# Kernel optimization log

Measured on AMD Instinct MI355X. Metric: run time of the kernel, lower is better.

Reference implementation:

```python
import jax, jax.numpy as jnp
import numpy as np

B, D, H = 16384, 1024, 4096


def setup_inputs() -> dict:
    key = jax.random.key(0)
    kx, kp, k1, k2 = jax.random.split(key, 4)
    X = jax.random.normal(kx, (B, D), dtype=jnp.float32)
    prot_col_idx = 3
    # protected column must be binary {0,1} so the remap produces no NaNs
    prot = jax.random.randint(kp, (B,), 0, 2).astype(jnp.float32)
    X = X.at[:, prot_col_idx].set(prot)
    W1 = jax.random.normal(k1, (D, H), dtype=jnp.float32) * (1.0 / np.sqrt(D))
    b1 = jnp.zeros((H,), dtype=jnp.float32)
    W2 = jax.random.normal(k2, (H, D), dtype=jnp.float32) * (1.0 / np.sqrt(H))
    b2 = jnp.zeros((D,), dtype=jnp.float32)
    return {"X": X, "W1": W1, "b1": b1, "W2": W2, "b2": b2,
            "prot_col_idx": prot_col_idx}


def reference(X, W1, b1, W2, b2, prot_col_idx):
    def explainer(x):
        h = jnp.tanh(x @ W1 + b1)          # [B, H]
        return h @ W2 + b2                  # [B, D]

    # vectorized remap of the protected column: 0 -> 1, 1 -> 0, else NaN
    col = X[:, prot_col_idx]
    flipped = jnp.where(col == 0, jnp.float32(1.0),
                        jnp.where(col == 1, jnp.float32(0.0), jnp.float32(jnp.nan)))
    X_copy = X.at[:, prot_col_idx].set(flipped.astype(X.dtype))

    shaps = explainer(X)
    shaps_counter = explainer(X_copy)
    mean_euclid_dist = jnp.mean(jnp.abs(shaps - shaps_counter), axis=0)  # [D]
    return mean_euclid_dist.sum()
```

## Files before the change

kernel.cpp:

```cpp
#include <hip/hip_runtime.h>
#include <stdint.h>

#define B_N 16384
#define D_N 1024
#define H_N 4096

typedef int i32x4 __attribute__((ext_vector_type(4)));
typedef int i32x8 __attribute__((ext_vector_type(8)));
typedef float f32x4 __attribute__((ext_vector_type(4)));

__device__ __forceinline__ void gload16(const void* g, void* l) {
  __builtin_amdgcn_global_load_lds((const __attribute__((address_space(1))) void*)g,
                                   (__attribute__((address_space(3))) void*)l,
                                   16, 0, 0);
}

__device__ __forceinline__ unsigned char f2fp8(float v) {
  return (unsigned char)(__builtin_amdgcn_cvt_pk_fp8_f32(v, v, 0, false) & 0xFF);
}

__global__ void pack_X_kernel(const float4* __restrict__ X4,
                              int* __restrict__ Xb,
                              float* __restrict__ s,
                              const int* __restrict__ pci_p) {
  int i = blockIdx.x * 256 + threadIdx.x;
  if (i >= B_N * (D_N / 4)) return;
  float4 v = X4[i];
  int p = __builtin_amdgcn_cvt_pk_fp8_f32(v.x, v.y, 0, false);
  p = __builtin_amdgcn_cvt_pk_fp8_f32(v.z, v.w, p, true);
  Xb[i] = p;
  int pci = *pci_p;
  int colg = i & (D_N / 4 - 1);
  if (colg == (pci >> 2)) {
    int row = i >> 8;
    float c;
    switch (pci & 3) {
      case 0:  c = v.x; break;
      case 1:  c = v.y; break;
      case 2:  c = v.z; break;
      default: c = v.w; break;
    }
    s[row] = 1.0f - 2.0f * c;
  }
}

__global__ void transpose_pack_fp8(const float* __restrict__ in,
                                   unsigned char* __restrict__ out,
                                   int R, int C, float scale,
                                   float* __restrict__ w3,
                                   const int* __restrict__ pci_p) {
  __shared__ float tile[32][33];
  int i0 = blockIdx.y * 32;
  int j0 = blockIdx.x * 32;
  int tx = threadIdx.x, ty = threadIdx.y;
  int pci = pci_p ? *pci_p : -1;
#pragma unroll
  for (int r = 0; r < 32; r += 8) {
    int i = i0 + ty + r;
    int j = j0 + tx;
    float v = in[(size_t)i * C + j];
    tile[ty + r][tx] = v;
    if (w3 != nullptr && i == pci) w3[j] = v;
  }
  __syncthreads();
#pragma unroll
  for (int r = 0; r < 32; r += 8) {
    int jo = j0 + ty + r;
    int io = i0 + tx;
    out[(size_t)jo * R + io] = f2fp8(tile[tx][ty + r] * scale);
  }
}

template <int KTOT>
__device__ __forceinline__ void mx_mainloop(
    const unsigned char* __restrict__ A, const unsigned char* __restrict__ B,
    int m0, int n0, int sa, int sb,
    unsigned char* As, unsigned char* Bs, f32x4 (&acc)[4][4]) {
  const int tid = threadIdx.x;
  const int lane = tid & 63;
  const int wave = tid >> 6;
  const int wm = (wave >> 1) * 64;
  const int wn = (wave & 1) * 64;
  const int lm = lane & 15;
  const int quad = lane >> 4;

  const int srow = tid >> 3;
  const int clog = (tid & 7) ^ (srow & 7);
  const unsigned char* Ag = A + (size_t)(m0 + srow) * KTOT + clog * 16;
  const unsigned char* Bg = B + (size_t)(n0 + srow) * KTOT + clog * 16;
  unsigned char* As_l = As + tid * 16;
  unsigned char* Bs_l = Bs + tid * 16;

  for (int k0 = 0; k0 < KTOT; k0 += 128) {
#pragma unroll
    for (int it = 0; it < 4; it++) {
      gload16(Ag + k0 + (size_t)(32 * it) * KTOT, As_l + it * 4096);
      gload16(Bg + k0 + (size_t)(32 * it) * KTOT, Bs_l + it * 4096);
    }
    __syncthreads();
    i32x8 a[4], b[4];
#pragma unroll
    for (int i = 0; i < 4; i++) {
      int r = wm + i * 16 + lm;
      int e = r & 7;
      i32x4 lo = *(const i32x4*)&As[r * 128 + ((2 * quad) ^ e) * 16];
      i32x4 hi = *(const i32x4*)&As[r * 128 + ((2 * quad + 1) ^ e) * 16];
      a[i][0] = lo[0]; a[i][1] = lo[1]; a[i][2] = lo[2]; a[i][3] = lo[3];
      a[i][4] = hi[0]; a[i][5] = hi[1]; a[i][6] = hi[2]; a[i][7] = hi[3];
    }
#pragma unroll
    for (int j = 0; j < 4; j++) {
      int r = wn + j * 16 + lm;
      int e = r & 7;
      i32x4 lo = *(const i32x4*)&Bs[r * 128 + ((2 * quad) ^ e) * 16];
      i32x4 hi = *(const i32x4*)&Bs[r * 128 + ((2 * quad + 1) ^ e) * 16];
      b[j][0] = lo[0]; b[j][1] = lo[1]; b[j][2] = lo[2]; b[j][3] = lo[3];
      b[j][4] = hi[0]; b[j][5] = hi[1]; b[j][6] = hi[2]; b[j][7] = hi[3];
    }
#pragma unroll
    for (int i = 0; i < 4; i++)
#pragma unroll
      for (int j = 0; j < 4; j++)
        acc[i][j] = __builtin_amdgcn_mfma_scale_f32_16x16x128_f8f6f4(
            a[i], b[j], acc[i][j], 0, 0, 0, sa, 0, sb);
    __syncthreads();
  }
}

__device__ __forceinline__ void xcd_remap(int NT, int MT, int& m_t, int& n_t) {
  int l = blockIdx.y * NT + blockIdx.x;
  int x = l & 7;
  int k = l >> 3;
  m_t = x * (MT >> 3) + k / NT;
  n_t = k % NT;
}

__global__ __launch_bounds__(256) void gemm1_dh(
    const unsigned char* __restrict__ Xb,
    const unsigned char* __restrict__ W1T,
    const float* __restrict__ b1,
    const float* __restrict__ w3,
    const float* __restrict__ s,
    unsigned char* __restrict__ Dh) {
  __shared__ alignas(16) unsigned char As[128 * 128];
  __shared__ alignas(16) unsigned char Bs[128 * 128];
  int m_t, n_t;
  xcd_remap(H_N / 128, B_N / 128, m_t, n_t);
  const int m0 = m_t * 128, n0 = n_t * 128;

  f32x4 acc[4][4] = {};
  mx_mainloop<D_N>(Xb, W1T, m0, n0, 127, 123, As, Bs, acc);

  const int tid = threadIdx.x;
  const int lane = tid & 63;
  const int wave = tid >> 6;
  const int wm = (wave >> 1) * 64;
  const int wn = (wave & 1) * 64;
  const int lm = lane & 15;
  const int quad = lane >> 4;

  float ewp[4], ewm[4], b1v[4];
  int ghv[4];
#pragma unroll
  for (int j = 0; j < 4; j++) {
    int gh = n0 + wn + j * 16 + lm;
    float w = w3[gh];
    ewp[j] = __expf(2.0f * w);
    ewm[j] = __expf(-2.0f * w);
    b1v[j] = b1[gh];
    ghv[j] = gh;
  }
#pragma unroll
  for (int i = 0; i < 4; i++) {
#pragma unroll
    for (int r = 0; r < 4; r++) {
      int gb = m0 + wm + i * 16 + quad * 4 + r;
      float sv = s[gb];
      size_t rowbase = (size_t)gb * H_N;
#pragma unroll
      for (int j = 0; j < 4; j++) {
        float z = acc[i][j][r] + b1v[j];
        z = fminf(fmaxf(z, -20.0f), 20.0f);
        float E = __expf(2.0f * z);
        float ews = (sv > 0.0f) ? ewp[j] : ewm[j];
        float num = 2.0f * E * (1.0f - ews);
        float den = (E * ews + 1.0f) * (E + 1.0f);
        float dh = num * __builtin_amdgcn_rcpf(den);
        Dh[rowbase + ghv[j]] = f2fp8(dh * 64.0f);
      }
    }
  }
}

__global__ __launch_bounds__(256) void gemm2_abs(
    const unsigned char* __restrict__ Dh,
    const unsigned char* __restrict__ W2T,
    float* __restrict__ accum) {
  __shared__ alignas(16) unsigned char As[128 * 128];
  __shared__ alignas(16) unsigned char Bs[128 * 128];
  __shared__ float wsum[4];
  int m_t, n_t;
  xcd_remap(D_N / 128, B_N / 128, m_t, n_t);
  const int m0 = m_t * 128, n0 = n_t * 128;

  f32x4 acc[4][4] = {};
  mx_mainloop<H_N>(Dh, W2T, m0, n0, 121, 121, As, Bs, acc);

  const int tid = threadIdx.x;
  const int lane = tid & 63;
  const int wave = tid >> 6;

  float t = 0.0f;
#pragma unroll
  for (int i = 0; i < 4; i++)
#pragma unroll
    for (int j = 0; j < 4; j++)
#pragma unroll
      for (int r = 0; r < 4; r++)
        t += fabsf(acc[i][j][r]);

#pragma unroll
  for (int off2 = 32; off2 > 0; off2 >>= 1)
    t += __shfl_down(t, off2, 64);
  if (lane == 0) wsum[wave] = t;
  __syncthreads();
  if (tid == 0) atomicAdd(accum, wsum[0] + wsum[1] + wsum[2] + wsum[3]);
}

__global__ void finalize_kernel(const float* __restrict__ acc, float* __restrict__ out) {
  out[0] = acc[0] * (1.0f / (float)B_N);
}

extern "C" void kernel_launch(void* const* d_in, const int* in_sizes, int n_in,
                              void* d_out, int out_size, void* d_ws, size_t ws_size,
                              hipStream_t stream) {
  const float* X  = (const float*)d_in[0];
  const float* W1 = (const float*)d_in[1];
  const float* b1 = (const float*)d_in[2];
  const float* W2 = (const float*)d_in[3];
  const int* pci  = (const int*)d_in[5];

  char* ws = (char*)d_ws;
  size_t off = 0;
  unsigned char* Xb  = (unsigned char*)(ws + off); off += (size_t)B_N * D_N;
  unsigned char* W1T = (unsigned char*)(ws + off); off += (size_t)H_N * D_N;
  unsigned char* W2T = (unsigned char*)(ws + off); off += (size_t)D_N * H_N;
  float* w3  = (float*)(ws + off); off += (size_t)H_N * 4;
  float* s   = (float*)(ws + off); off += (size_t)B_N * 4;
  float* acc = (float*)(ws + off); off += 256;
  unsigned char* Dh  = (unsigned char*)(ws + off); off += (size_t)B_N * H_N;
  if (ws_size < off) return;

  hipMemsetAsync(acc, 0, sizeof(float), stream);
  pack_X_kernel<<<B_N * (D_N / 4) / 256, 256, 0, stream>>>((const float4*)X, (int*)Xb, s, pci);
  transpose_pack_fp8<<<dim3(H_N / 32, D_N / 32), dim3(32, 8), 0, stream>>>(W1, W1T, D_N, H_N, 16.0f, w3, pci);
  transpose_pack_fp8<<<dim3(D_N / 32, H_N / 32), dim3(32, 8), 0, stream>>>(W2, W2T, H_N, D_N, 64.0f, nullptr, nullptr);
  gemm1_dh<<<dim3(H_N / 128, B_N / 128), 256, 0, stream>>>(Xb, W1T, b1, w3, s, Dh);
  gemm2_abs<<<dim3(D_N / 128, B_N / 128), 256, 0, stream>>>(Dh, W2T, acc);
  finalize_kernel<<<1, 1, 0, stream>>>(acc, (float*)d_out);
}
```

Before: 326.4 us.

## Merge prep kernels, retile GEMM block mapping, simplify epilogue, drop finalize

Fuses the X packing and both weight transposes into one prep kernel, which cuts launch overhead and lets the three jobs share the GPU. Changes the block-to-tile mapping in both GEMMs so tiles are grouped per XCD for better L2 reuse. Simplifies the tanh-difference epilogue: the scale is folded into precomputed numerators, the clamp is one-sided at 12, and outputs are converted to fp8 in pairs. Removes the finalize kernel by scaling each block's partial sum before the atomic add into the output. The one-sided clamp depends on a large negative z making E underflow to zero harmlessly.

```diff
diff --git a/kernel.cpp b/kernel.cpp
--- a/kernel.cpp
+++ b/kernel.cpp
@@ -19,41 +19,11 @@
   return (unsigned char)(__builtin_amdgcn_cvt_pk_fp8_f32(v, v, 0, false) & 0xFF);
 }
 
-__global__ void pack_X_kernel(const float4* __restrict__ X4,
-                              int* __restrict__ Xb,
-                              float* __restrict__ s,
-                              const int* __restrict__ pci_p) {
-  int i = blockIdx.x * 256 + threadIdx.x;
-  if (i >= B_N * (D_N / 4)) return;
-  float4 v = X4[i];
-  int p = __builtin_amdgcn_cvt_pk_fp8_f32(v.x, v.y, 0, false);
-  p = __builtin_amdgcn_cvt_pk_fp8_f32(v.z, v.w, p, true);
-  Xb[i] = p;
-  int pci = *pci_p;
-  int colg = i & (D_N / 4 - 1);
-  if (colg == (pci >> 2)) {
-    int row = i >> 8;
-    float c;
-    switch (pci & 3) {
-      case 0:  c = v.x; break;
-      case 1:  c = v.y; break;
-      case 2:  c = v.z; break;
-      default: c = v.w; break;
-    }
-    s[row] = 1.0f - 2.0f * c;
-  }
-}
-
-__global__ void transpose_pack_fp8(const float* __restrict__ in,
-                                   unsigned char* __restrict__ out,
-                                   int R, int C, float scale,
-                                   float* __restrict__ w3,
-                                   const int* __restrict__ pci_p) {
+__device__ __forceinline__ void transpose_tile(
+    const float* __restrict__ in, unsigned char* __restrict__ out,
+    int R, int C, float scale, float* __restrict__ w3, int pci,
+    int i0, int j0, int tx, int ty) {
   __shared__ float tile[32][33];
-  int i0 = blockIdx.y * 32;
-  int j0 = blockIdx.x * 32;
-  int tx = threadIdx.x, ty = threadIdx.y;
-  int pci = pci_p ? *pci_p : -1;
 #pragma unroll
   for (int r = 0; r < 32; r += 8) {
     int i = i0 + ty + r;
@@ -68,6 +38,44 @@
     int jo = j0 + ty + r;
     int io = i0 + tx;
     out[(size_t)jo * R + io] = f2fp8(tile[tx][ty + r] * scale);
+  }
+}
+
+__global__ __launch_bounds__(256) void prep_kernel(
+    const float4* __restrict__ X4, int* __restrict__ Xb,
+    float* __restrict__ s,
+    const float* __restrict__ W1, unsigned char* __restrict__ W1T, float* __restrict__ w3,
+    const float* __restrict__ W2, unsigned char* __restrict__ W2T,
+    const int* __restrict__ pci_p) {
+  int b = blockIdx.x;
+  int tid = threadIdx.x;
+  int pci = *pci_p;
+  if (b < 16384) {
+    int i = b * 256 + tid;
+    float4 v = X4[i];
+    int p = __builtin_amdgcn_cvt_pk_fp8_f32(v.x, v.y, 0, false);
+    p = __builtin_amdgcn_cvt_pk_fp8_f32(v.z, v.w, p, true);
+    Xb[i] = p;
+    int colg = i & (D_N / 4 - 1);
+    if (colg == (pci >> 2)) {
+      int row = i >> 8;
+      float c;
+      switch (pci & 3) {
+        case 0:  c = v.x; break;
+        case 1:  c = v.y; break;
+        case 2:  c = v.z; break;
+        default: c = v.w; break;
+      }
+      s[row] = 1.0f - 2.0f * c;
+    }
+  } else if (b < 20480) {
+    int id = b - 16384;
+    transpose_tile(W1, W1T, D_N, H_N, 16.0f, w3, pci,
+                   (id >> 7) * 32, (id & 127) * 32, tid & 31, tid >> 5);
+  } else {
+    int id = b - 20480;
+    transpose_tile(W2, W2T, H_N, D_N, 64.0f, nullptr, -1,
+                   (id >> 5) * 32, (id & 31) * 32, tid & 31, tid >> 5);
   }
 }
 
@@ -127,14 +135,6 @@
   }
 }
 
-__device__ __forceinline__ void xcd_remap(int NT, int MT, int& m_t, int& n_t) {
-  int l = blockIdx.y * NT + blockIdx.x;
-  int x = l & 7;
-  int k = l >> 3;
-  m_t = x * (MT >> 3) + k / NT;
-  n_t = k % NT;
-}
-
 __global__ __launch_bounds__(256) void gemm1_dh(
     const unsigned char* __restrict__ Xb,
     const unsigned char* __restrict__ W1T,
@@ -144,9 +144,16 @@
     unsigned char* __restrict__ Dh) {
   __shared__ alignas(16) unsigned char As[128 * 128];
   __shared__ alignas(16) unsigned char Bs[128 * 128];
-  int m_t, n_t;
-  xcd_remap(H_N / 128, B_N / 128, m_t, n_t);
-  const int m0 = m_t * 128, n0 = n_t * 128;
+  {
+  }
+  int l = blockIdx.y * gridDim.x + blockIdx.x;
+  int x = l & 7;
+  int k = l >> 3;
+  int ni = k & 7;
+  int m  = (k >> 3) & 15;
+  int nc = k >> 7;
+  const int m0 = (x * 16 + m) * 128;
+  const int n0 = (nc * 8 + ni) * 128;
 
   f32x4 acc[4][4] = {};
   mx_mainloop<D_N>(Xb, W1T, m0, n0, 127, 123, As, Bs, acc);
@@ -159,14 +166,17 @@
   const int lm = lane & 15;
   const int quad = lane >> 4;
 
-  float ewp[4], ewm[4], b1v[4];
+  float ewp[4], ewm[4], nump[4], numm[4], b1v[4];
   int ghv[4];
 #pragma unroll
   for (int j = 0; j < 4; j++) {
     int gh = n0 + wn + j * 16 + lm;
     float w = w3[gh];
-    ewp[j] = __expf(2.0f * w);
-    ewm[j] = __expf(-2.0f * w);
+    float ep = __expf(2.0f * w);
+    float em = __expf(-2.0f * w);
+    ewp[j] = ep; ewm[j] = em;
+    nump[j] = 128.0f * (1.0f - ep);
+    numm[j] = 128.0f * (1.0f - em);
     b1v[j] = b1[gh];
     ghv[j] = gh;
   }
@@ -175,19 +185,24 @@
 #pragma unroll
     for (int r = 0; r < 4; r++) {
       int gb = m0 + wm + i * 16 + quad * 4 + r;
-      float sv = s[gb];
+      bool sp = s[gb] > 0.0f;
       size_t rowbase = (size_t)gb * H_N;
+      float o[4];
 #pragma unroll
       for (int j = 0; j < 4; j++) {
-        float z = acc[i][j][r] + b1v[j];
-        z = fminf(fmaxf(z, -20.0f), 20.0f);
+        float ews = sp ? ewp[j] : ewm[j];
+        float num = sp ? nump[j] : numm[j];
+        float z = fminf(acc[i][j][r] + b1v[j], 12.0f);
         float E = __expf(2.0f * z);
-        float ews = (sv > 0.0f) ? ewp[j] : ewm[j];
-        float num = 2.0f * E * (1.0f - ews);
         float den = (E * ews + 1.0f) * (E + 1.0f);
-        float dh = num * __builtin_amdgcn_rcpf(den);
-        Dh[rowbase + ghv[j]] = f2fp8(dh * 64.0f);
+        o[j] = (E * num) * __builtin_amdgcn_rcpf(den);
       }
+      int p01 = __builtin_amdgcn_cvt_pk_fp8_f32(o[0], o[1], 0, false);
+      int p23 = __builtin_amdgcn_cvt_pk_fp8_f32(o[2], o[3], 0, false);
+      Dh[rowbase + ghv[0]] = (unsigned char)(p01 & 0xFF);
+      Dh[rowbase + ghv[1]] = (unsigned char)((p01 >> 8) & 0xFF);
+      Dh[rowbase + ghv[2]] = (unsigned char)(p23 & 0xFF);
+      Dh[rowbase + ghv[3]] = (unsigned char)((p23 >> 8) & 0xFF);
     }
   }
 }
@@ -195,13 +210,17 @@
 __global__ __launch_bounds__(256) void gemm2_abs(
     const unsigned char* __restrict__ Dh,
     const unsigned char* __restrict__ W2T,
-    float* __restrict__ accum) {
+    float* __restrict__ out) {
   __shared__ alignas(16) unsigned char As[128 * 128];
   __shared__ alignas(16) unsigned char Bs[128 * 128];
   __shared__ float wsum[4];
-  int m_t, n_t;
-  xcd_remap(D_N / 128, B_N / 128, m_t, n_t);
-  const int m0 = m_t * 128, n0 = n_t * 128;
+  int l = blockIdx.y * gridDim.x + blockIdx.x;
+  int x = l & 7;
+  int k = l >> 3;
+  int ni = k & 7;
+  int m  = k >> 3;
+  const int m0 = (x * 16 + m) * 128;
+  const int n0 = ni * 128;
 
   f32x4 acc[4][4] = {};
   mx_mainloop<H_N>(Dh, W2T, m0, n0, 121, 121, As, Bs, acc);
@@ -224,11 +243,8 @@
     t += __shfl_down(t, off2, 64);
   if (lane == 0) wsum[wave] = t;
   __syncthreads();
-  if (tid == 0) atomicAdd(accum, wsum[0] + wsum[1] + wsum[2] + wsum[3]);
-}
-
-__global__ void finalize_kernel(const float* __restrict__ acc, float* __restrict__ out) {
-  out[0] = acc[0] * (1.0f / (float)B_N);
+  if (tid == 0)
+    atomicAdd(out, (wsum[0] + wsum[1] + wsum[2] + wsum[3]) * (1.0f / (float)B_N));
 }
 
 extern "C" void kernel_launch(void* const* d_in, const int* in_sizes, int n_in,
@@ -247,15 +263,12 @@
   unsigned char* W2T = (unsigned char*)(ws + off); off += (size_t)D_N * H_N;
   float* w3  = (float*)(ws + off); off += (size_t)H_N * 4;
   float* s   = (float*)(ws + off); off += (size_t)B_N * 4;
-  float* acc = (float*)(ws + off); off += 256;
   unsigned char* Dh  = (unsigned char*)(ws + off); off += (size_t)B_N * H_N;
   if (ws_size < off) return;
 
-  hipMemsetAsync(acc, 0, sizeof(float), stream);
-  pack_X_kernel<<<B_N * (D_N / 4) / 256, 256, 0, stream>>>((const float4*)X, (int*)Xb, s, pci);
-  transpose_pack_fp8<<<dim3(H_N / 32, D_N / 32), dim3(32, 8), 0, stream>>>(W1, W1T, D_N, H_N, 16.0f, w3, pci);
-  transpose_pack_fp8<<<dim3(D_N / 32, H_N / 32), dim3(32, 8), 0, stream>>>(W2, W2T, H_N, D_N, 64.0f, nullptr, nullptr);
-  gemm1_dh<<<dim3(H_N / 128, B_N / 128), 256, 0, stream>>>(Xb, W1T, b1, w3, s, Dh);
-  gemm2_abs<<<dim3(D_N / 128, B_N / 128), 256, 0, stream>>>(Dh, W2T, acc);
-  finalize_kernel<<<1, 1, 0, stream>>>(acc, (float*)d_out);
-}
+  hipMemsetAsync(d_out, 0, sizeof(float), stream);
+  prep_kernel<<<24576, 256, 0, stream>>>((const float4*)X, (int*)Xb, s,
+                                         W1, W1T, w3, W2, W2T, pci);
+  gemm1_dh<<<dim3(32, 128), 256, 0, stream>>>(Xb, W1T, b1, w3, s, Dh);
+  gemm2_abs<<<dim3(8, 128), 256, 0, stream>>>(Dh, W2T, (float*)d_out);
+}
```

New measurement: 310.7 us. -4.8%, faster.
